# Performance work log

Hardware: AMD Instinct MI355X
Metric: run time of the kernel (lower is better)

## Reference

```python
import jax, jax.numpy as jnp
import numpy as np

B, S, D = 8, 2048, 1024
EPS = 1e-5


def setup_inputs() -> dict:
    key = jax.random.key(0)
    ks = jax.random.split(key, 8)
    s = 1.0 / np.sqrt(D)
    return {
        "x": jax.random.normal(ks[0], (B, S, D), dtype=jnp.float32),
        "Wq": jax.random.normal(ks[1], (D, D), dtype=jnp.float32) * s,
        "bq": jnp.zeros((D,), dtype=jnp.float32),
        "Wk": jax.random.normal(ks[2], (D, D), dtype=jnp.float32) * s,
        "bk": jnp.zeros((D,), dtype=jnp.float32),
        "Wv": jax.random.normal(ks[3], (D, D), dtype=jnp.float32) * s,
        "bv": jnp.zeros((D,), dtype=jnp.float32),
        "gamma": jnp.ones((D,), dtype=jnp.float32),
        "beta": jnp.zeros((D,), dtype=jnp.float32),
    }


def reference(x, Wq, bq, Wk, bk, Wv, bv, gamma, beta):
    # Linear layers (torch convention: y = x @ W^T + b)
    Q = jnp.einsum('bsd,ed->bse', x, Wq) + bq
    K = jnp.einsum('bsd,ed->bse', x, Wk) + bk
    V = jnp.einsum('bsd,ed->bse', x, Wv) + bv
    scale = 1.0 / jnp.sqrt(jnp.asarray(D, dtype=x.dtype))
    scores = jnp.einsum('bqd,bkd->bqk', Q, K) * scale  # [B,S,S]
    attn = jax.nn.softmax(scores, axis=-1)
    out = jnp.einsum('bqk,bkd->bqd', attn, V) + x  # attention + residual
    # LayerNorm over last dim
    mu = jnp.mean(out, axis=-1, keepdims=True)
    var = jnp.var(out, axis=-1, keepdims=True)
    return (out - mu) * jax.lax.rsqrt(var + EPS) * gamma + beta
```

## Files before the change

kernel.cpp:

```cpp
#include <hip/hip_runtime.h>


typedef __bf16 bf16x8 __attribute__((ext_vector_type(8)));
typedef float f32x4 __attribute__((ext_vector_type(4)));

enum { M_QKV = 0, M_SC = 1, M_PV = 2 };

__device__ __forceinline__ unsigned short f2b(float f) {
  union { float f; unsigned int u; } v; v.f = f;
  return (unsigned short)((v.u + 0x7FFFu + ((v.u >> 16) & 1u)) >> 16);
}

#define GL16(gsrc, ldst)                                         \
  __builtin_amdgcn_global_load_lds(                              \
      (const __attribute__((address_space(1))) void*)(gsrc),     \
      (__attribute__((address_space(3))) void*)(ldst), 16, 0, 0)

__device__ __forceinline__ void stage_tile(
    const unsigned short* Ab, const unsigned short* Bb, char* lds,
    int b, int tau, int gm0, int gn0, int ldaE, int ldbE, int t)
{
  const int kc = tau << 6;
  const int row4 = t >> 3;
  const int c = (t & 7) << 4;
  const int wb = (t & ~63) * 16;
#pragma unroll
  for (int r = 0; r < 4; ++r) {
    const int row = r * 64 + row4;
    const int cs = c ^ ((row & 12) << 3);
    GL16((const char*)(Ab + (size_t)(gm0 + row) * ldaE + kc) + cs,
         lds + b * 65536 + r * 8192 + wb);
    __builtin_amdgcn_sched_barrier(0);
  }
#pragma unroll
  for (int r = 0; r < 4; ++r) {
    const int row = r * 64 + row4;
    const int cs = c ^ ((row & 12) << 3);
    GL16((const char*)(Bb + (size_t)(gn0 + row) * ldbE + kc) + cs,
         lds + b * 65536 + 32768 + r * 8192 + wb);
    __builtin_amdgcn_sched_barrier(0);
  }
}

__device__ __forceinline__ bf16x8 ldsrd(const char* lds, int base, int row, int kb) {
  int p = row * 128 + kb;
  p ^= (p & 0x600) >> 4;
  return *(const bf16x8*)(lds + base + p);
}

template <int MODE>
__global__ __launch_bounds__(512, 2) void gemm8(
    const unsigned short* __restrict__ A, const unsigned short* __restrict__ B,
    void* __restrict__ C0, void* __restrict__ C1, void* __restrict__ C2,
    const float* __restrict__ x0, const float* __restrict__ x1,
    const float* __restrict__ x2,
    int K, int ldaE, int ldbE, size_t sA, size_t sB)
{
  extern __shared__ char lds[];
  const int t = threadIdx.x, l = t & 63, w = t >> 6;
  const int bz = blockIdx.z;
  const unsigned short* Ab = A + (size_t)bz * sA;
  const unsigned short* Bb = B + (size_t)bz * sB;
  const int gm0 = blockIdx.y * 256, gn0 = blockIdx.x * 256;
  const int lo16 = l & 15, hi4 = l >> 4;
  const int kb0 = hi4 * 16;
  const int nt = K >> 6;

  f32x4 acc[2][16];
#pragma unroll
  for (int i = 0; i < 2; ++i)
#pragma unroll
    for (int j = 0; j < 16; ++j) acc[i][j] = f32x4{0.f, 0.f, 0.f, 0.f};

  stage_tile(Ab, Bb, lds, 0, 0, gm0, gn0, ldaE, ldbE, t);

  bf16x8 af[2][2];
  for (int tau = 0; tau < nt; ++tau) {
    const int abase = (tau & 1) * 65536, bbase = abase + 32768;
    const bool more = (tau + 1) < nt;
    asm volatile("s_waitcnt vmcnt(3)" ::: "memory");
    __builtin_amdgcn_sched_barrier(0);
    __builtin_amdgcn_s_barrier();
    __builtin_amdgcn_sched_barrier(0);
    if (more)
      stage_tile(Ab, Bb, lds, (tau & 1) ^ 1, tau + 1, gm0, gn0, ldaE, ldbE, t);
    bf16x8 bf[4][2];
#pragma unroll
    for (int mf = 0; mf < 2; ++mf)
#pragma unroll
      for (int ks = 0; ks < 2; ++ks)
        af[mf][ks] = ldsrd(lds, abase, w * 32 + mf * 16 + lo16, ks * 64 + kb0);
#pragma unroll
    for (int nf = 0; nf < 4; ++nf)
#pragma unroll
      for (int ks = 0; ks < 2; ++ks)
        bf[nf][ks] = ldsrd(lds, bbase, nf * 16 + lo16, ks * 64 + kb0);
    asm volatile("s_waitcnt lgkmcnt(0)" ::: "memory");
    __builtin_amdgcn_sched_barrier(0);
    __builtin_amdgcn_s_setprio(1);
#pragma unroll
    for (int mf = 0; mf < 2; ++mf)
#pragma unroll
      for (int nf = 0; nf < 4; ++nf)
#pragma unroll
        for (int ks = 0; ks < 2; ++ks)
          acc[mf][nf] = __builtin_amdgcn_mfma_f32_16x16x32_bf16(
              af[mf][ks], bf[nf][ks], acc[mf][nf], 0, 0, 0);
    __builtin_amdgcn_s_setprio(0);
#pragma unroll
    for (int p = 1; p < 4; ++p) {
      if (p == 1) {
        if (more) asm volatile("s_waitcnt vmcnt(10)" ::: "memory");
        else      asm volatile("s_waitcnt vmcnt(2)" ::: "memory");
      } else if (p == 2) {
        if (more) asm volatile("s_waitcnt vmcnt(9)" ::: "memory");
        else      asm volatile("s_waitcnt vmcnt(1)" ::: "memory");
      } else {
        if (more) asm volatile("s_waitcnt vmcnt(8)" ::: "memory");
        else      asm volatile("s_waitcnt vmcnt(0)" ::: "memory");
      }
      __builtin_amdgcn_sched_barrier(0);
      __builtin_amdgcn_s_barrier();
      __builtin_amdgcn_sched_barrier(0);
#pragma unroll
      for (int nf = 0; nf < 4; ++nf)
#pragma unroll
        for (int ks = 0; ks < 2; ++ks)
          bf[nf][ks] = ldsrd(lds, bbase, (p * 4 + nf) * 16 + lo16, ks * 64 + kb0);
      asm volatile("s_waitcnt lgkmcnt(0)" ::: "memory");
      __builtin_amdgcn_sched_barrier(0);
      __builtin_amdgcn_s_setprio(1);
#pragma unroll
      for (int mf = 0; mf < 2; ++mf)
#pragma unroll
        for (int nf = 0; nf < 4; ++nf)
#pragma unroll
          for (int ks = 0; ks < 2; ++ks)
            acc[mf][p * 4 + nf] = __builtin_amdgcn_mfma_f32_16x16x32_bf16(
                af[mf][ks], bf[nf][ks], acc[mf][p * 4 + nf], 0, 0, 0);
      __builtin_amdgcn_s_setprio(0);
    }
  }

#pragma unroll
  for (int mf = 0; mf < 2; ++mf) {
    const int grow = gm0 + w * 32 + mf * 16 + hi4 * 4;
#pragma unroll
    for (int nf = 0; nf < 16; ++nf) {
      const int gc = gn0 + nf * 16 + lo16;
      if constexpr (MODE == M_QKV) {
        if (gc < 1024) {
          unsigned short* Q = (unsigned short*)C0;
          const float b = x0[gc];
#pragma unroll
          for (int r = 0; r < 4; ++r)
            Q[(size_t)(grow + r) * 1024 + gc] = f2b(acc[mf][nf][r] + b);
        } else if (gc < 2048) {
          unsigned short* Kk = (unsigned short*)C1;
          const float b = x1[gc - 1024];
#pragma unroll
          for (int r = 0; r < 4; ++r)
            Kk[(size_t)(grow + r) * 1024 + (gc - 1024)] = f2b(acc[mf][nf][r] + b);
        } else {
          unsigned short* Vt = (unsigned short*)C2;
          const float b = x2[gc - 2048];
          const int bat = grow >> 11, lm = grow & 2047;
          ushort4 o = make_ushort4(
              f2b(acc[mf][nf][0] + b), f2b(acc[mf][nf][1] + b),
              f2b(acc[mf][nf][2] + b), f2b(acc[mf][nf][3] + b));
          *(ushort4*)&Vt[(size_t)bat * 2097152 + (size_t)(gc - 2048) * 2048 + lm] = o;
        }
      } else if constexpr (MODE == M_SC) {
        float* C = (float*)C0 + (size_t)bz * 4194304;
        float* p = C + (size_t)grow * 2048 + gc;
#pragma unroll
        for (int r = 0; r < 4; ++r) p[(size_t)r * 2048] = acc[mf][nf][r] * 0.03125f;
      } else {
        float* C = (float*)C0 + (size_t)bz * 2097152;
        const float* R = x0 + (size_t)bz * 2097152;
        float* p = C + (size_t)grow * 1024 + gc;
        const float* q = R + (size_t)grow * 1024 + gc;
#pragma unroll
        for (int r = 0; r < 4; ++r) p[(size_t)r * 1024] = acc[mf][nf][r] + q[(size_t)r * 1024];
      }
    }
  }
}

__global__ __launch_bounds__(256) void f32_to_bf16(
    const float* __restrict__ s, unsigned short* __restrict__ d)
{
  const size_t i = (size_t)blockIdx.x * 256 + threadIdx.x;
  const float4 a = ((const float4*)s)[i * 2];
  const float4 b = ((const float4*)s)[i * 2 + 1];
  ((ushort4*)d)[i * 2]     = make_ushort4(f2b(a.x), f2b(a.y), f2b(a.z), f2b(a.w));
  ((ushort4*)d)[i * 2 + 1] = make_ushort4(f2b(b.x), f2b(b.y), f2b(b.z), f2b(b.w));
}

__global__ __launch_bounds__(256) void softmax2048_bf16(float* __restrict__ S)
{
  __shared__ float redm[4];
  __shared__ float reds[4];
  const int t = threadIdx.x;
  float* p = S + (size_t)blockIdx.x * 2048;
  float4 a = *(const float4*)&p[t * 4];
  float4 b = *(const float4*)&p[t * 4 + 1024];
  float m = fmaxf(fmaxf(fmaxf(a.x, a.y), fmaxf(a.z, a.w)),
                  fmaxf(fmaxf(b.x, b.y), fmaxf(b.z, b.w)));
#pragma unroll
  for (int o = 32; o; o >>= 1) m = fmaxf(m, __shfl_xor(m, o));
  if ((t & 63) == 0) redm[t >> 6] = m;
  __syncthreads();
  m = fmaxf(fmaxf(redm[0], redm[1]), fmaxf(redm[2], redm[3]));
  a.x = __expf(a.x - m); a.y = __expf(a.y - m);
  a.z = __expf(a.z - m); a.w = __expf(a.w - m);
  b.x = __expf(b.x - m); b.y = __expf(b.y - m);
  b.z = __expf(b.z - m); b.w = __expf(b.w - m);
  float s = a.x + a.y + a.z + a.w + b.x + b.y + b.z + b.w;
#pragma unroll
  for (int o = 32; o; o >>= 1) s += __shfl_xor(s, o);
  if ((t & 63) == 0) reds[t >> 6] = s;
  __syncthreads();
  s = reds[0] + reds[1] + reds[2] + reds[3];
  const float inv = 1.0f / s;
  unsigned short* pb = (unsigned short*)p;
  *(ushort4*)&pb[t * 4] =
      make_ushort4(f2b(a.x * inv), f2b(a.y * inv), f2b(a.z * inv), f2b(a.w * inv));
  *(ushort4*)&pb[1024 + t * 4] =
      make_ushort4(f2b(b.x * inv), f2b(b.y * inv), f2b(b.z * inv), f2b(b.w * inv));
}

__global__ __launch_bounds__(64) void ln1024(
    float* __restrict__ O, const float* __restrict__ g, const float* __restrict__ be)
{
  const int l = threadIdx.x;
  float* p = O + (size_t)blockIdx.x * 1024;
  float4 v[4];
#pragma unroll
  for (int i = 0; i < 4; ++i) v[i] = *(const float4*)&p[l * 4 + i * 256];
  float s = 0.f, q = 0.f;
#pragma unroll
  for (int i = 0; i < 4; ++i) {
    s += v[i].x + v[i].y + v[i].z + v[i].w;
    q += v[i].x * v[i].x + v[i].y * v[i].y + v[i].z * v[i].z + v[i].w * v[i].w;
  }
#pragma unroll
  for (int o = 32; o; o >>= 1) { s += __shfl_xor(s, o); q += __shfl_xor(q, o); }
  const float mu = s * (1.0f / 1024.0f);
  const float var = q * (1.0f / 1024.0f) - mu * mu;
  const float rs = rsqrtf(var + 1e-5f);
#pragma unroll
  for (int i = 0; i < 4; ++i) {
    const float4 gg = *(const float4*)&g[l * 4 + i * 256];
    const float4 bb = *(const float4*)&be[l * 4 + i * 256];
    float4 o4;
    o4.x = (v[i].x - mu) * rs * gg.x + bb.x;
    o4.y = (v[i].y - mu) * rs * gg.y + bb.y;
    o4.z = (v[i].z - mu) * rs * gg.z + bb.z;
    o4.w = (v[i].w - mu) * rs * gg.w + bb.w;
    *(float4*)&p[l * 4 + i * 256] = o4;
  }
}

extern "C" void kernel_launch(void* const* d_in, const int* in_sizes, int n_in,
                              void* d_out, int out_size, void* d_ws, size_t ws_size,
                              hipStream_t stream) {
  (void)in_sizes; (void)n_in; (void)out_size; (void)ws_size;
  constexpr int Bb = 8, S = 2048, D = 1024;
  const size_t BS = (size_t)Bb * S;
  const size_t ND = BS * (size_t)D;

  const float* x     = (const float*)d_in[0];
  const float* Wq    = (const float*)d_in[1];
  const float* bq    = (const float*)d_in[2];
  const float* Wk    = (const float*)d_in[3];
  const float* bk    = (const float*)d_in[4];
  const float* Wv    = (const float*)d_in[5];
  const float* bv    = (const float*)d_in[6];
  const float* gamma = (const float*)d_in[7];
  const float* beta  = (const float*)d_in[8];
  float* out = (float*)d_out;

  unsigned short* xb = (unsigned short*)d_ws;
  unsigned short* Qb = xb + ND;
  unsigned short* Kb = Qb + ND;
  unsigned short* Vt = Kb + ND;
  float* Sbuf = (float*)(Vt + ND);
  unsigned short* Wcat = (unsigned short*)Sbuf;

  hipFuncSetAttribute((const void*)gemm8<M_QKV>,
                      hipFuncAttributeMaxDynamicSharedMemorySize, 131072);
  hipFuncSetAttribute((const void*)gemm8<M_SC>,
                      hipFuncAttributeMaxDynamicSharedMemorySize, 131072);
  hipFuncSetAttribute((const void*)gemm8<M_PV>,
                      hipFuncAttributeMaxDynamicSharedMemorySize, 131072);

  f32_to_bf16<<<dim3(8192), dim3(256), 0, stream>>>(x, xb);
  f32_to_bf16<<<dim3(512), dim3(256), 0, stream>>>(Wq, Wcat);
  f32_to_bf16<<<dim3(512), dim3(256), 0, stream>>>(Wk, Wcat + (size_t)D * D);
  f32_to_bf16<<<dim3(512), dim3(256), 0, stream>>>(Wv, Wcat + 2 * (size_t)D * D);

  gemm8<M_QKV><<<dim3(12, 64, 1), dim3(512), 131072, stream>>>(
      xb, Wcat, Qb, Kb, Vt, bq, bk, bv, D, D, D, 0, 0);
  gemm8<M_SC><<<dim3(8, 8, 8), dim3(512), 131072, stream>>>(
      Qb, Kb, Sbuf, nullptr, nullptr, nullptr, nullptr, nullptr,
      D, D, D, (size_t)S * D, (size_t)S * D);
  softmax2048_bf16<<<dim3((int)BS), dim3(256), 0, stream>>>(Sbuf);
  gemm8<M_PV><<<dim3(4, 8, 8), dim3(512), 131072, stream>>>(
      (const unsigned short*)Sbuf, Vt, out, nullptr, nullptr, x, nullptr, nullptr,
      S, 2 * S, S, (size_t)S * 2 * S, (size_t)D * S);
  ln1024<<<dim3((int)BS), dim3(64), 0, stream>>>(out, gamma, beta);
}
```

Measured before the change: 523.9 us.

## Retile GEMM warps to 2x4 grid with fragment-ordered LDS layout

Switches the warp tiling in the bf16 MFMA GEMM from each wave owning 32 rows by all 256 columns to a 2x4 wave grid where each wave owns 128x64. The LDS layout is rearranged so each 16x32 fragment is stored contiguously in lane order, which makes LDS reads linear with no swizzle. The k-step is split into four quadrant phases, which reduces LDS read traffic per MFMA and cuts per-step barriers from four to three. The costs are more live A/B fragment registers and global loads that land already in MFMA fragment order, so global access is less coalesced.

Measured after the change: 518.5 us. Within noise of the previous version (-1.0%).

```diff
diff --git a/kernel.cpp b/kernel.cpp
--- a/kernel.cpp
+++ b/kernel.cpp
@@ -15,38 +15,6 @@
   __builtin_amdgcn_global_load_lds(                              \
       (const __attribute__((address_space(1))) void*)(gsrc),     \
       (__attribute__((address_space(3))) void*)(ldst), 16, 0, 0)
-
-__device__ __forceinline__ void stage_tile(
-    const unsigned short* Ab, const unsigned short* Bb, char* lds,
-    int b, int tau, int gm0, int gn0, int ldaE, int ldbE, int t)
-{
-  const int kc = tau << 6;
-  const int row4 = t >> 3;
-  const int c = (t & 7) << 4;
-  const int wb = (t & ~63) * 16;
-#pragma unroll
-  for (int r = 0; r < 4; ++r) {
-    const int row = r * 64 + row4;
-    const int cs = c ^ ((row & 12) << 3);
-    GL16((const char*)(Ab + (size_t)(gm0 + row) * ldaE + kc) + cs,
-         lds + b * 65536 + r * 8192 + wb);
-    __builtin_amdgcn_sched_barrier(0);
-  }
-#pragma unroll
-  for (int r = 0; r < 4; ++r) {
-    const int row = r * 64 + row4;
-    const int cs = c ^ ((row & 12) << 3);
-    GL16((const char*)(Bb + (size_t)(gn0 + row) * ldbE + kc) + cs,
-         lds + b * 65536 + 32768 + r * 8192 + wb);
-    __builtin_amdgcn_sched_barrier(0);
-  }
-}
-
-__device__ __forceinline__ bf16x8 ldsrd(const char* lds, int base, int row, int kb) {
-  int p = row * 128 + kb;
-  p ^= (p & 0x600) >> 4;
-  return *(const bf16x8*)(lds + base + p);
-}
 
 template <int MODE>
 __global__ __launch_bounds__(512, 2) void gemm8(
@@ -58,130 +26,178 @@
 {
   extern __shared__ char lds[];
   const int t = threadIdx.x, l = t & 63, w = t >> 6;
+  const int wm = w >> 2, wn = w & 3;
+  const int rl = l & 15, hi4 = l >> 4;
+  const int cl8 = hi4 * 8;
   const int bz = blockIdx.z;
   const unsigned short* Ab = A + (size_t)bz * sA;
   const unsigned short* Bb = B + (size_t)bz * sB;
   const int gm0 = blockIdx.y * 256, gn0 = blockIdx.x * 256;
-  const int lo16 = l & 15, hi4 = l >> 4;
-  const int kb0 = hi4 * 16;
   const int nt = K >> 6;
 
-  f32x4 acc[2][16];
-#pragma unroll
-  for (int i = 0; i < 2; ++i)
-#pragma unroll
-    for (int j = 0; j < 16; ++j) acc[i][j] = f32x4{0.f, 0.f, 0.f, 0.f};
-
-  stage_tile(Ab, Bb, lds, 0, 0, gm0, gn0, ldaE, ldbE, t);
-
-  bf16x8 af[2][2];
+  const int frA0 = (w & 3) + (w >> 2) * 8;
+  const int frB0 = (w >> 1) * 4 + (w & 1);
+
+  const unsigned short* sp[8];
+  int ub[8];
+  sp[0] = Ab + (size_t)(gm0 + frA0 * 16 + rl) * ldaE + cl8;
+  sp[1] = sp[0] + 32;
+  sp[2] = Bb + (size_t)(gn0 + frB0 * 16 + rl) * ldbE + cl8;
+  sp[3] = sp[2] + 32;
+  sp[4] = Bb + (size_t)(gn0 + (frB0 + 2) * 16 + rl) * ldbE + cl8;
+  sp[5] = sp[4] + 32;
+  sp[6] = Ab + (size_t)(gm0 + (frA0 + 4) * 16 + rl) * ldaE + cl8;
+  sp[7] = sp[6] + 32;
+  ub[0] = frA0 * 2048;             ub[1] = ub[0] + 1024;
+  ub[2] = 32768 + frB0 * 2048;     ub[3] = ub[2] + 1024;
+  ub[4] = 32768 + (frB0 + 2) * 2048; ub[5] = ub[4] + 1024;
+  ub[6] = (frA0 + 4) * 2048;       ub[7] = ub[6] + 1024;
+
+  auto stage = [&](int tau, int buf) {
+#pragma unroll
+    for (int s = 0; s < 8; ++s) {
+      GL16(sp[s] + (size_t)tau * 64, lds + buf * 65536 + ub[s]);
+      __builtin_amdgcn_sched_barrier(0);
+    }
+  };
+
+  f32x4 acc[8][4];
+#pragma unroll
+  for (int i = 0; i < 8; ++i)
+#pragma unroll
+    for (int j = 0; j < 4; ++j) acc[i][j] = f32x4{0.f, 0.f, 0.f, 0.f};
+
+  stage(0, 0);
+
+  const int lb = l * 16;
+  bf16x8 a[4][2], b0[2][2], b1[2][2];
+
   for (int tau = 0; tau < nt; ++tau) {
-    const int abase = (tau & 1) * 65536, bbase = abase + 32768;
+    const char* bp = lds + (tau & 1) * 65536;
     const bool more = (tau + 1) < nt;
-    asm volatile("s_waitcnt vmcnt(3)" ::: "memory");
+    asm volatile("s_waitcnt vmcnt(4)" ::: "memory");
     __builtin_amdgcn_sched_barrier(0);
     __builtin_amdgcn_s_barrier();
     __builtin_amdgcn_sched_barrier(0);
-    if (more)
-      stage_tile(Ab, Bb, lds, (tau & 1) ^ 1, tau + 1, gm0, gn0, ldaE, ldbE, t);
-    bf16x8 bf[4][2];
-#pragma unroll
-    for (int mf = 0; mf < 2; ++mf)
+    if (more) stage(tau + 1, (tau & 1) ^ 1);
+#pragma unroll
+    for (int mf = 0; mf < 4; ++mf)
 #pragma unroll
       for (int ks = 0; ks < 2; ++ks)
-        af[mf][ks] = ldsrd(lds, abase, w * 32 + mf * 16 + lo16, ks * 64 + kb0);
-#pragma unroll
-    for (int nf = 0; nf < 4; ++nf)
+        a[mf][ks] = *(const bf16x8*)(bp + ((wm * 8 + mf) * 2 + ks) * 1024 + lb);
+#pragma unroll
+    for (int nf = 0; nf < 2; ++nf)
 #pragma unroll
       for (int ks = 0; ks < 2; ++ks)
-        bf[nf][ks] = ldsrd(lds, bbase, nf * 16 + lo16, ks * 64 + kb0);
+        b0[nf][ks] = *(const bf16x8*)(bp + 32768 + ((wn * 4 + nf) * 2 + ks) * 1024 + lb);
     asm volatile("s_waitcnt lgkmcnt(0)" ::: "memory");
     __builtin_amdgcn_sched_barrier(0);
     __builtin_amdgcn_s_setprio(1);
 #pragma unroll
-    for (int mf = 0; mf < 2; ++mf)
-#pragma unroll
-      for (int nf = 0; nf < 4; ++nf)
+    for (int mf = 0; mf < 4; ++mf)
+#pragma unroll
+      for (int nf = 0; nf < 2; ++nf)
 #pragma unroll
         for (int ks = 0; ks < 2; ++ks)
           acc[mf][nf] = __builtin_amdgcn_mfma_f32_16x16x32_bf16(
-              af[mf][ks], bf[nf][ks], acc[mf][nf], 0, 0, 0);
+              a[mf][ks], b0[nf][ks], acc[mf][nf], 0, 0, 0);
     __builtin_amdgcn_s_setprio(0);
-#pragma unroll
-    for (int p = 1; p < 4; ++p) {
-      if (p == 1) {
-        if (more) asm volatile("s_waitcnt vmcnt(10)" ::: "memory");
-        else      asm volatile("s_waitcnt vmcnt(2)" ::: "memory");
-      } else if (p == 2) {
-        if (more) asm volatile("s_waitcnt vmcnt(9)" ::: "memory");
-        else      asm volatile("s_waitcnt vmcnt(1)" ::: "memory");
-      } else {
-        if (more) asm volatile("s_waitcnt vmcnt(8)" ::: "memory");
-        else      asm volatile("s_waitcnt vmcnt(0)" ::: "memory");
-      }
-      __builtin_amdgcn_sched_barrier(0);
-      __builtin_amdgcn_s_barrier();
-      __builtin_amdgcn_sched_barrier(0);
-#pragma unroll
-      for (int nf = 0; nf < 4; ++nf)
+    if (more) asm volatile("s_waitcnt vmcnt(10)" ::: "memory");
+    else      asm volatile("s_waitcnt vmcnt(2)"  ::: "memory");
+    __builtin_amdgcn_sched_barrier(0);
+    __builtin_amdgcn_s_barrier();
+    __builtin_amdgcn_sched_barrier(0);
+#pragma unroll
+    for (int nf = 0; nf < 2; ++nf)
+#pragma unroll
+      for (int ks = 0; ks < 2; ++ks)
+        b1[nf][ks] = *(const bf16x8*)(bp + 32768 + ((wn * 4 + 2 + nf) * 2 + ks) * 1024 + lb);
+    asm volatile("s_waitcnt lgkmcnt(0)" ::: "memory");
+    __builtin_amdgcn_sched_barrier(0);
+    __builtin_amdgcn_s_setprio(1);
+#pragma unroll
+    for (int mf = 0; mf < 4; ++mf)
+#pragma unroll
+      for (int nf = 0; nf < 2; ++nf)
 #pragma unroll
         for (int ks = 0; ks < 2; ++ks)
-          bf[nf][ks] = ldsrd(lds, bbase, (p * 4 + nf) * 16 + lo16, ks * 64 + kb0);
-      asm volatile("s_waitcnt lgkmcnt(0)" ::: "memory");
-      __builtin_amdgcn_sched_barrier(0);
-      __builtin_amdgcn_s_setprio(1);
-#pragma unroll
-      for (int mf = 0; mf < 2; ++mf)
-#pragma unroll
-        for (int nf = 0; nf < 4; ++nf)
-#pragma unroll
-          for (int ks = 0; ks < 2; ++ks)
-            acc[mf][p * 4 + nf] = __builtin_amdgcn_mfma_f32_16x16x32_bf16(
-                af[mf][ks], bf[nf][ks], acc[mf][p * 4 + nf], 0, 0, 0);
-      __builtin_amdgcn_s_setprio(0);
-    }
+          acc[mf][2 + nf] = __builtin_amdgcn_mfma_f32_16x16x32_bf16(
+              a[mf][ks], b1[nf][ks], acc[mf][2 + nf], 0, 0, 0);
+    __builtin_amdgcn_s_setprio(0);
+    if (more) asm volatile("s_waitcnt vmcnt(8)" ::: "memory");
+    else      asm volatile("s_waitcnt vmcnt(0)" ::: "memory");
+    __builtin_amdgcn_sched_barrier(0);
+    __builtin_amdgcn_s_barrier();
+    __builtin_amdgcn_sched_barrier(0);
+#pragma unroll
+    for (int mf = 0; mf < 4; ++mf)
+#pragma unroll
+      for (int ks = 0; ks < 2; ++ks)
+        a[mf][ks] = *(const bf16x8*)(bp + ((wm * 8 + 4 + mf) * 2 + ks) * 1024 + lb);
+    asm volatile("s_waitcnt lgkmcnt(0)" ::: "memory");
+    __builtin_amdgcn_sched_barrier(0);
+    __builtin_amdgcn_s_setprio(1);
+#pragma unroll
+    for (int mf = 0; mf < 4; ++mf)
+#pragma unroll
+      for (int nf = 0; nf < 2; ++nf)
+#pragma unroll
+        for (int ks = 0; ks < 2; ++ks)
+          acc[4 + mf][2 + nf] = __builtin_amdgcn_mfma_f32_16x16x32_bf16(
+              a[mf][ks], b1[nf][ks], acc[4 + mf][2 + nf], 0, 0, 0);
+    __builtin_amdgcn_s_setprio(0);
+    __builtin_amdgcn_s_setprio(1);
+#pragma unroll
+    for (int mf = 0; mf < 4; ++mf)
+#pragma unroll
+      for (int nf = 0; nf < 2; ++nf)
+#pragma unroll
+        for (int ks = 0; ks < 2; ++ks)
+          acc[4 + mf][nf] = __builtin_amdgcn_mfma_f32_16x16x32_bf16(
+              a[mf][ks], b0[nf][ks], acc[4 + mf][nf], 0, 0, 0);
+    __builtin_amdgcn_s_setprio(0);
   }
 
 #pragma unroll
-  for (int mf = 0; mf < 2; ++mf) {
-    const int grow = gm0 + w * 32 + mf * 16 + hi4 * 4;
-#pragma unroll
-    for (int nf = 0; nf < 16; ++nf) {
-      const int gc = gn0 + nf * 16 + lo16;
+  for (int Mf = 0; Mf < 8; ++Mf) {
+    const int grow = gm0 + wm * 128 + Mf * 16 + hi4 * 4;
+#pragma unroll
+    for (int Nf = 0; Nf < 4; ++Nf) {
+      const int gc = gn0 + wn * 64 + Nf * 16 + rl;
       if constexpr (MODE == M_QKV) {
         if (gc < 1024) {
           unsigned short* Q = (unsigned short*)C0;
           const float b = x0[gc];
 #pragma unroll
           for (int r = 0; r < 4; ++r)
-            Q[(size_t)(grow + r) * 1024 + gc] = f2b(acc[mf][nf][r] + b);
+            Q[(size_t)(grow + r) * 1024 + gc] = f2b(acc[Mf][Nf][r] + b);
         } else if (gc < 2048) {
           unsigned short* Kk = (unsigned short*)C1;
           const float b = x1[gc - 1024];
 #pragma unroll
           for (int r = 0; r < 4; ++r)
-            Kk[(size_t)(grow + r) * 1024 + (gc - 1024)] = f2b(acc[mf][nf][r] + b);
+            Kk[(size_t)(grow + r) * 1024 + (gc - 1024)] = f2b(acc[Mf][Nf][r] + b);
         } else {
           unsigned short* Vt = (unsigned short*)C2;
           const float b = x2[gc - 2048];
           const int bat = grow >> 11, lm = grow & 2047;
           ushort4 o = make_ushort4(
-              f2b(acc[mf][nf][0] + b), f2b(acc[mf][nf][1] + b),
-              f2b(acc[mf][nf][2] + b), f2b(acc[mf][nf][3] + b));
+              f2b(acc[Mf][Nf][0] + b), f2b(acc[Mf][Nf][1] + b),
+              f2b(acc[Mf][Nf][2] + b), f2b(acc[Mf][Nf][3] + b));
           *(ushort4*)&Vt[(size_t)bat * 2097152 + (size_t)(gc - 2048) * 2048 + lm] = o;
         }
       } else if constexpr (MODE == M_SC) {
         float* C = (float*)C0 + (size_t)bz * 4194304;
         float* p = C + (size_t)grow * 2048 + gc;
 #pragma unroll
-        for (int r = 0; r < 4; ++r) p[(size_t)r * 2048] = acc[mf][nf][r] * 0.03125f;
+        for (int r = 0; r < 4; ++r) p[(size_t)r * 2048] = acc[Mf][Nf][r] * 0.03125f;
       } else {
         float* C = (float*)C0 + (size_t)bz * 2097152;
         const float* R = x0 + (size_t)bz * 2097152;
         float* p = C + (size_t)grow * 1024 + gc;
         const float* q = R + (size_t)grow * 1024 + gc;
 #pragma unroll
-        for (int r = 0; r < 4; ++r) p[(size_t)r * 1024] = acc[mf][nf][r] + q[(size_t)r * 1024];
+        for (int r = 0; r < 4; ++r) p[(size_t)r * 1024] = acc[Mf][Nf][r] + q[(size_t)r * 1024];
       }
     }
   }
```
